# Performance work log

Measured on AMD Instinct MI355X. Metric: run time of the kernel, lower is better.

## Reference

```python
import jax, jax.numpy as jnp
import numpy as np

B, N, D = 64, 256, 768
ITER_STEPS = 1


def _linear_w(key, out_d, in_d):
    s = 1.0 / np.sqrt(in_d)
    return jax.random.uniform(key, (out_d, in_d), jnp.float32, -s, s)


def setup_inputs() -> dict:
    key = jax.random.key(0)
    ks = jax.random.split(key, 16)
    node = jax.random.normal(ks[0], (B, N, D), jnp.float32)
    node_mask = jnp.ones((B, N), jnp.int32)
    argument_graph = jax.random.randint(ks[1], (B, N, N), 0, 2, jnp.int32)
    punctuation_graph = jax.random.randint(ks[2], (B, N, N), 0, 2, jnp.int32)
    inp = {
        "node": node,
        "node_mask": node_mask,
        "argument_graph": argument_graph,
        "punctuation_graph": punctuation_graph,
        # node-relatedness scorer: Linear(D, 1, bias=True)
        "Wq": _linear_w(ks[3], 1, D),
        "bq": jnp.zeros((1,), jnp.float32),
        # self node fc: Linear(D, D, bias=True)
        "Ws": _linear_w(ks[4], D, D),
        "bs": jnp.zeros((D,), jnp.float32),
        # 8 relation projections, Linear(D, D, bias=False)
        "Wa": _linear_w(ks[5], D, D),
        "Wp": _linear_w(ks[6], D, D),
        "Wap": _linear_w(ks[7], D, D),
        "Wpp": _linear_w(ks[8], D, D),
        "Wa2": _linear_w(ks[9], D, D),
        "Wp2": _linear_w(ks[10], D, D),
        "Wap2": _linear_w(ks[11], D, D),
        "Wpp2": _linear_w(ks[12], D, D),
    }
    return inp


def reference(node, node_mask, argument_graph, punctuation_graph,
              Wq, bq, Ws, bs, Wa, Wp, Wap, Wpp, Wa2, Wp2, Wap2, Wpp2):
    f32 = jnp.float32
    mask = node_mask.astype(f32)                      # [B, N]
    n = node.shape[1]
    eye = jnp.eye(n, dtype=f32)
    # dd_graph: node_mask outer product with zeroed diagonal
    dd = mask[:, None, :] * mask[:, :, None] * (1.0 - eye)   # [B, N, N]
    g_a = dd * argument_graph.astype(f32)
    g_p = dd * punctuation_graph.astype(f32)
    # reverse directed edges
    g_ar = dd * jnp.swapaxes(g_a, 1, 2)
    g_pr = dd * jnp.swapaxes(g_p, 1, 2)
    neigh = g_a.sum(-1) + g_p.sum(-1) + g_ar.sum(-1) + g_pr.sum(-1)  # [B, N]
    denom = jnp.where(neigh >= 1.0, neigh, 1.0)

    all_weight = []
    for _ in range(ITER_STEPS):
        # (1) node relatedness
        dw = jax.nn.sigmoid(jnp.einsum('bnd,od->bno', node, Wq) + bq)[..., 0]  # [B, N]
        all_weight.append(dw)
        self_info = jnp.einsum('bnd,ed->bne', node, Ws) + bs

        def msg(g, W):
            # node_weight: broadcast dw over rows, zero where no edge
            nw = dw[:, None, :] * g                    # [B, N, N]
            proj = jnp.einsum('bnd,ed->bne', node, W)  # [B, N, D]
            return jnp.matmul(nw, proj)                # [B, N, D]

        agg = (msg(g_a, Wa) + msg(g_p, Wp) + msg(g_ar, Wap) + msg(g_pr, Wpp)
               + msg(g_a, Wa2) + msg(g_p, Wp2) + msg(g_ar, Wap2) + msg(g_pr, Wpp2))
        agg = agg / denom[..., None]
        # (3) node update
        node = jax.nn.relu(self_info + agg)

    all_weight = jnp.stack(all_weight, axis=1)  # [B, steps, N]
    return node, all_weight
```

## Files before the change

### kernel.cpp

```cpp
#include <hip/hip_runtime.h>
#include <hip/hip_bf16.h>
#include <math.h>

typedef __bf16 bf16;
typedef unsigned char u8;
typedef unsigned long long ull;
typedef __bf16 bf16x8 __attribute__((ext_vector_type(8)));
typedef float f32x4 __attribute__((ext_vector_type(4)));

#define BB 64
#define NN 256
#define DD 768
#define MM (BB*NN)
#define KP 1024
#define WSZ (DD*DD)
#define TL2 272
#define AROW2 196608


__device__ __forceinline__ void async16(const void* g, void* l) {
  __builtin_amdgcn_global_load_lds((__attribute__((address_space(1))) void*)g,
                                   (__attribute__((address_space(3))) void*)l,
                                   16, 0, 0);
}

__device__ __forceinline__ void stage_tile(const bf16* gsrc, int ld, char* ldst,
                                           int wv, int lane) {
#pragma unroll
  for (int cc = 0; cc < 2; ++cc) {
    int c = wv * 2 + cc;
    int row = c * 16 + (lane >> 2);
    int col = (lane & 3) * 8;
    async16(gsrc + (size_t)row * ld + col, ldst + c * 1024);
  }
}

__device__ __forceinline__ void mma_step(const char* lA, const char* lB,
                                         f32x4 acc[4][4], int lane, int wr, int wc) {
  bf16x8 af[4], bfr[4];
  int rbase = wr * 64 + (lane & 15);
  int cbase = wc * 64 + (lane & 15);
  int ko = (lane >> 4) * 8;
#pragma unroll
  for (int r = 0; r < 4; ++r)
    af[r] = *(const bf16x8*)(lA + (((rbase + r * 16) * 32) + ko) * 2);
#pragma unroll
  for (int c = 0; c < 4; ++c)
    bfr[c] = *(const bf16x8*)(lB + (((cbase + c * 16) * 32) + ko) * 2);
#pragma unroll
  for (int r = 0; r < 4; ++r)
#pragma unroll
    for (int c = 0; c < 4; ++c)
      acc[r][c] = __builtin_amdgcn_mfma_f32_16x16x32_bf16(af[r], bfr[c], acc[r][c], 0, 0, 0);
}

__device__ __forceinline__ void mma_step_fp8t(const char* lA, const char* lB,
                                              f32x4 acc[4][4], int lane, int wr, int wc) {
  long af[4], bfr[4];
  int koq = (lane >> 4) * 1024;
  int mA = (wr * 64 + (lane & 15)) * 8;
  int mB = (wc * 64 + (lane & 15)) * 8;
#pragma unroll
  for (int r = 0; r < 4; ++r)
    af[r] = *(const long*)(lA + koq + mA + r * 128);
#pragma unroll
  for (int c = 0; c < 4; ++c)
    bfr[c] = *(const long*)(lB + koq + mB + c * 128);
#pragma unroll
  for (int r = 0; r < 4; ++r)
#pragma unroll
    for (int c = 0; c < 4; ++c)
      acc[r][c] = __builtin_amdgcn_mfma_f32_16x16x32_fp8_fp8(af[r], bfr[c], acc[r][c], 0, 0, 0);
}

__device__ __forceinline__ void k_step64(const bf16* Ab, int lda, const bf16* Bb, int ldb,
                                         char* smem, f32x4 acc[4][4],
                                         int wv, int lane, int wr, int wc) {
  char* lA0 = smem;
  char* lA1 = smem + 8192;
  char* lB0 = smem + 16384;
  char* lB1 = smem + 24576;
  __syncthreads();
  stage_tile(Ab, lda, lA0, wv, lane);
  stage_tile(Ab + 32, lda, lA1, wv, lane);
  stage_tile(Bb, ldb, lB0, wv, lane);
  stage_tile(Bb + 32, ldb, lB1, wv, lane);
  __builtin_amdgcn_s_waitcnt(0);
  __syncthreads();
  mma_step(lA0, lB0, acc, lane, wr, wc);
  mma_step(lA1, lB1, acc, lane, wr, wc);
}

__device__ __forceinline__ unsigned pack4(float a, float b, float c, float d) {
  int w = 0;
  w = __builtin_amdgcn_cvt_pk_fp8_f32(a, b, w, false);
  w = __builtin_amdgcn_cvt_pk_fp8_f32(c, d, w, true);
  return (unsigned)w;
}

__global__ void k_pre(const float* __restrict__ node, const float* __restrict__ Wq,
                      const float* __restrict__ bq, bf16* __restrict__ node_bf,
                      float* __restrict__ dw, float* __restrict__ allw,
                      float* __restrict__ neigh,
                      const float* __restrict__ Ws,
                      const float* __restrict__ Wa, const float* __restrict__ Wp,
                      const float* __restrict__ Wap, const float* __restrict__ Wpp,
                      const float* __restrict__ Wa2, const float* __restrict__ Wp2,
                      const float* __restrict__ Wap2, const float* __restrict__ Wpp2,
                      bf16* __restrict__ Wcat4, bf16* __restrict__ Ws_bf) {
  if (blockIdx.x < MM / 4) {
    int lane = threadIdx.x & 63, wv = threadIdx.x >> 6;
    int row = blockIdx.x * 4 + wv;
    const float* nr = node + (size_t)row * DD;
    bf16* nb = node_bf + (size_t)row * DD;
    float s = 0.f;
#pragma unroll
    for (int k = 0; k < DD / 64; ++k) {
      int idx = lane + k * 64;
      float v = nr[idx];
      nb[idx] = (bf16)v;
      s += v * Wq[idx];
    }
#pragma unroll
    for (int off = 32; off; off >>= 1) s += __shfl_down(s, off);
    if (lane == 0) {
      float z = s + bq[0];
      float d = 1.f / (1.f + expf(-z));
      dw[row] = d;
      allw[row] = d;
      neigh[row] = 0.f;
    }
  } else {
    int i = (blockIdx.x - MM / 4) * 256 + threadIdx.x;
    Ws_bf[i] = (bf16)Ws[i];
    Wcat4[i]           = (bf16)(Wa[i] + Wa2[i]);
    Wcat4[i + WSZ]     = (bf16)(Wp[i] + Wp2[i]);
    Wcat4[i + 2 * WSZ] = (bf16)(Wap[i] + Wap2[i]);
    Wcat4[i + 3 * WSZ] = (bf16)(Wpp[i] + Wpp2[i]);
  }
}

__device__ __forceinline__ void store_tiled(u8* base, int tile, int kin, int m, uint4 v) {
  size_t o = (size_t)tile * 4096 + (size_t)((kin >> 3) * 1024 + m * 8);
  *(ull*)(base + o)        = ((ull)v.y << 32) | v.x;
  *(ull*)(base + o + 1024) = ((ull)v.w << 32) | v.z;
}

__global__ void k_graph(const int* __restrict__ mask, const int* __restrict__ arg,
                        const int* __restrict__ pun, const float* __restrict__ dw,
                        u8* __restrict__ g8, float* __restrict__ neigh) {
  __shared__ float la[64][65];
  __shared__ float lp[64][65];
  __shared__ float msk[256];
  __shared__ float dwv[256];
  int tid = threadIdx.x;
  int bi = blockIdx.x;
  int b = bi >> 4, it = (bi >> 2) & 3, jt = bi & 3;
  int i0 = it * 64, j0 = jt * 64;
  msk[tid] = (float)mask[b * NN + tid];
  dwv[tid] = dw[b * NN + tid];
  __syncthreads();
  int ir = tid >> 2, c4 = (tid & 3) * 16;
  int i = i0 + ir;
  float mi = msk[i];
  size_t gb = (size_t)b * NN * NN;
  const int* ap = arg + gb + (size_t)i * NN + j0 + c4;
  const int* pp = pun + gb + (size_t)i * NN + j0 + c4;
  float va[16], vp[16];
  float racc = 0.f;
#pragma unroll
  for (int k = 0; k < 16; ++k) {
    int j = j0 + c4 + k;
    float dd = (i == j) ? 0.f : mi * msk[j];
    float ga = dd * (float)ap[k];
    float gp = dd * (float)pp[k];
    la[ir][c4 + k] = ga;
    lp[ir][c4 + k] = gp;
    float w = dwv[j];
    va[k] = w * ga;
    vp[k] = w * gp;
    racc += ga + gp;
  }
  uint4 oa, op;
#pragma unroll
  for (int g = 0; g < 4; ++g) {
    (&oa.x)[g] = pack4(va[g*4], va[g*4+1], va[g*4+2], va[g*4+3]);
    (&op.x)[g] = pack4(vp[g*4], vp[g*4+1], vp[g*4+2], vp[g*4+3]);
  }
  {
    int tR = (b * 2 + (i >> 7)) * 32;
    int K0 = j0 + c4;
    store_tiled(g8, tR + (K0 >> 5),       K0 & 31, i & 127, oa);
    store_tiled(g8, tR + 8 + (K0 >> 5),   K0 & 31, i & 127, op);
  }
  racc += __shfl_xor(racc, 1);
  racc += __shfl_xor(racc, 2);
  if ((tid & 3) == 0) atomicAdd(&neigh[b * NN + i], racc);
  __syncthreads();
  int jr = ir, ic4 = c4;
  float cacc = 0.f;
#pragma unroll
  for (int k = 0; k < 16; ++k) {
    float ga = la[ic4 + k][jr];
    float gp = lp[ic4 + k][jr];
    float w = dwv[i0 + ic4 + k];
    va[k] = w * ga;
    vp[k] = w * gp;
    cacc += ga + gp;
  }
#pragma unroll
  for (int g = 0; g < 4; ++g) {
    (&oa.x)[g] = pack4(va[g*4], va[g*4+1], va[g*4+2], va[g*4+3]);
    (&op.x)[g] = pack4(vp[g*4], vp[g*4+1], vp[g*4+2], vp[g*4+3]);
  }
  {
    int row = j0 + jr;
    int tR = (b * 2 + (row >> 7)) * 32;
    int K2 = i0 + ic4;
    store_tiled(g8, tR + 16 + (K2 >> 5),  K2 & 31, row & 127, oa);
    store_tiled(g8, tR + 24 + (K2 >> 5),  K2 & 31, row & 127, op);
  }
  cacc += __shfl_xor(cacc, 1);
  cacc += __shfl_xor(cacc, 2);
  if ((tid & 3) == 0) atomicAdd(&neigh[b * NN + j0 + jr], cacc);
}

template<int T>
__device__ __forceinline__ void proj_ph(char* smem, int wvoff,
                                        const char* gA, const char* gB,
                                        int aoff, int boff,
                                        bf16x8 (&ca)[8], bf16x8 (&cb)[4],
                                        bf16x8 (&na)[8], bf16x8 (&nb)[4],
                                        f32x4 (&acc)[8][4]) {
  if constexpr (T <= 20)      asm volatile("s_waitcnt vmcnt(8)" ::: "memory");
  else if constexpr (T == 21) asm volatile("s_waitcnt vmcnt(4)" ::: "memory");
  else                        asm volatile("s_waitcnt vmcnt(0)" ::: "memory");
  __builtin_amdgcn_s_barrier();
  __builtin_amdgcn_sched_barrier(0);
  if constexpr (T + 4 < 24) {
    char* D = smem + (T & 3) * 32768 + wvoff;
    const char* sA = gA + (T + 4) * 64;
    const char* sB = gB + (T + 4) * 64;
    async16(sA,         D);
    async16(sA + AROW2, D + 8192);
    async16(sB,         D + 16384);
    async16(sB + AROW2, D + 24576);
  }
  if constexpr (T + 1 < 24) {
    const char* L = smem + ((T + 1) & 3) * 32768;
#pragma unroll
    for (int r = 0; r < 8; ++r) na[r] = *(const bf16x8*)(L + aoff + r * 1024);
#pragma unroll
    for (int c = 0; c < 4; ++c) nb[c] = *(const bf16x8*)(L + boff + c * 1024);
  }
  __builtin_amdgcn_s_setprio(1);
#pragma unroll
  for (int r = 0; r < 8; ++r)
#pragma unroll
    for (int c = 0; c < 4; ++c)
      acc[r][c] = __builtin_amdgcn_mfma_f32_16x16x32_bf16(ca[r], cb[c], acc[r][c], 0, 0, 0);
  __builtin_amdgcn_s_setprio(0);
  asm volatile("s_waitcnt lgkmcnt(0)" ::: "memory");
  __builtin_amdgcn_sched_barrier(0);
}

__global__ __launch_bounds__(512, 2) void k_proj(const bf16* __restrict__ node_bf,
                                                 const bf16* __restrict__ Wcat4,
                                                 u8* __restrict__ p8) {
  __shared__ __align__(16) char smem[131072];
  int tid = threadIdx.x, lane = tid & 63, wv = tid >> 6;
  int wr = wv >> 2, wc = wv & 3;
  int l = blockIdx.x, xcd = l & 7, idx = l >> 3;
  int b = (idx / 12) * 8 + xcd;
  int nt = idx % 12;
  int n0 = nt * 256;
  int m0 = b * 256;
  int srcS = (tid & 3) ^ ((tid >> 3) & 3);
  const char* gA = (const char*)node_bf + (size_t)m0 * 1536 + (tid >> 2) * 1536 + srcS * 16;
  const char* gB = (const char*)Wcat4  + (size_t)n0 * 1536 + (tid >> 2) * 1536 + srcS * 16;
  int wvoff = wv * 1024;
  int sSwR = ((lane >> 4) ^ (((lane & 15) >> 1) & 3)) << 4;
  int aoff = (wr * 128 + (lane & 15)) * 64 + sSwR;
  int boff = 16384 + (wc * 64 + (lane & 15)) * 64 + sSwR;
  f32x4 z = {0.f, 0.f, 0.f, 0.f};
  f32x4 acc[8][4];
#pragma unroll
  for (int r = 0; r < 8; ++r)
#pragma unroll
    for (int c = 0; c < 4; ++c) acc[r][c] = z;
  bf16x8 fa0[8], fb0[4], fa1[8], fb1[4];
#pragma unroll
  for (int u = 0; u < 4; ++u) {
    char* D = smem + u * 32768 + wvoff;
    const char* sA = gA + u * 64;
    const char* sB = gB + u * 64;
    async16(sA,         D);
    async16(sA + AROW2, D + 8192);
    async16(sB,         D + 16384);
    async16(sB + AROW2, D + 24576);
  }
  asm volatile("s_waitcnt vmcnt(12)" ::: "memory");
  __builtin_amdgcn_s_barrier();
  __builtin_amdgcn_sched_barrier(0);
#pragma unroll
  for (int r = 0; r < 8; ++r) fa0[r] = *(const bf16x8*)(smem + aoff + r * 1024);
#pragma unroll
  for (int c = 0; c < 4; ++c) fb0[c] = *(const bf16x8*)(smem + boff + c * 1024);
  asm volatile("s_waitcnt lgkmcnt(0)" ::: "memory");
  __builtin_amdgcn_sched_barrier(0);
  proj_ph< 0>(smem, wvoff, gA, gB, aoff, boff, fa0, fb0, fa1, fb1, acc);
  proj_ph< 1>(smem, wvoff, gA, gB, aoff, boff, fa1, fb1, fa0, fb0, acc);
  proj_ph< 2>(smem, wvoff, gA, gB, aoff, boff, fa0, fb0, fa1, fb1, acc);
  proj_ph< 3>(smem, wvoff, gA, gB, aoff, boff, fa1, fb1, fa0, fb0, acc);
  proj_ph< 4>(smem, wvoff, gA, gB, aoff, boff, fa0, fb0, fa1, fb1, acc);
  proj_ph< 5>(smem, wvoff, gA, gB, aoff, boff, fa1, fb1, fa0, fb0, acc);
  proj_ph< 6>(smem, wvoff, gA, gB, aoff, boff, fa0, fb0, fa1, fb1, acc);
  proj_ph< 7>(smem, wvoff, gA, gB, aoff, boff, fa1, fb1, fa0, fb0, acc);
  proj_ph< 8>(smem, wvoff, gA, gB, aoff, boff, fa0, fb0, fa1, fb1, acc);
  proj_ph< 9>(smem, wvoff, gA, gB, aoff, boff, fa1, fb1, fa0, fb0, acc);
  proj_ph<10>(smem, wvoff, gA, gB, aoff, boff, fa0, fb0, fa1, fb1, acc);
  proj_ph<11>(smem, wvoff, gA, gB, aoff, boff, fa1, fb1, fa0, fb0, acc);
  proj_ph<12>(smem, wvoff, gA, gB, aoff, boff, fa0, fb0, fa1, fb1, acc);
  proj_ph<13>(smem, wvoff, gA, gB, aoff, boff, fa1, fb1, fa0, fb0, acc);
  proj_ph<14>(smem, wvoff, gA, gB, aoff, boff, fa0, fb0, fa1, fb1, acc);
  proj_ph<15>(smem, wvoff, gA, gB, aoff, boff, fa1, fb1, fa0, fb0, acc);
  proj_ph<16>(smem, wvoff, gA, gB, aoff, boff, fa0, fb0, fa1, fb1, acc);
  proj_ph<17>(smem, wvoff, gA, gB, aoff, boff, fa1, fb1, fa0, fb0, acc);
  proj_ph<18>(smem, wvoff, gA, gB, aoff, boff, fa0, fb0, fa1, fb1, acc);
  proj_ph<19>(smem, wvoff, gA, gB, aoff, boff, fa1, fb1, fa0, fb0, acc);
  proj_ph<20>(smem, wvoff, gA, gB, aoff, boff, fa0, fb0, fa1, fb1, acc);
  proj_ph<21>(smem, wvoff, gA, gB, aoff, boff, fa1, fb1, fa0, fb0, acc);
  proj_ph<22>(smem, wvoff, gA, gB, aoff, boff, fa0, fb0, fa1, fb1, acc);
  proj_ph<23>(smem, wvoff, gA, gB, aoff, boff, fa1, fb1, fa0, fb0, acc);
  __syncthreads();
  u8* tb = (u8*)smem;
  int X = n0 / DD, e0 = n0 % DD;
#pragma unroll
  for (int r = 0; r < 8; ++r)
#pragma unroll
    for (int c = 0; c < 4; ++c) {
      int n = wc * 64 + c * 16 + (lane & 15);
      int m = wr * 128 + r * 16 + ((lane >> 4) << 2);
      *(unsigned*)(tb + n * TL2 + m) =
          pack4(acc[r][c][0], acc[r][c][1], acc[r][c][2], acc[r][c][3]);
    }
  __syncthreads();
#pragma unroll
  for (int t2 = 0; t2 < 8; ++t2) {
    int erow = t2 * 32 + (tid & 31);
    int col = (tid >> 5) * 16;
    uint4 v = *(const uint4*)(tb + erow * TL2 + col);
    int e = e0 + erow;
    int tR = (b * 6 + (e >> 7)) * 32 + X * 8;
    store_tiled(p8, tR + (col >> 5), col & 31, e & 127, v);
  }
}

__global__ __launch_bounds__(256) void k_agg(const u8* __restrict__ g8,
                                             const u8* __restrict__ p8,
                                             const bf16* __restrict__ node_bf,
                                             const bf16* __restrict__ Ws_bf,
                                             const float* __restrict__ neigh,
                                             const float* __restrict__ bs,
                                             float* __restrict__ out) {
  __shared__ __align__(16) char smem[32768];
  int tid = threadIdx.x, lane = tid & 63, wv = tid >> 6, wr = wv >> 1, wc = wv & 1;
  int l = blockIdx.x;
  int xcd = l & 7, idx = l >> 3;
  int b = (idx / 12) * 8 + xcd;
  int t = idx % 12;
  int i0 = (t / 6) * 128, e0 = (t % 6) * 128;
  f32x4 z = {0.f, 0.f, 0.f, 0.f};
  f32x4 acc[4][4];
#pragma unroll
  for (int r = 0; r < 4; ++r)
#pragma unroll
    for (int c = 0; c < 4; ++c) acc[r][c] = z;
  const u8* At = g8 + (size_t)((b * 2 + (i0 >> 7)) * 32) * 4096;
  const u8* Bt = p8 + (size_t)((b * 6 + (e0 >> 7)) * 32) * 4096;
  int lsoff = wv * 1024;
  int goff = lsoff + lane * 16;
  for (int k0 = 0; k0 < KP; k0 += 128) {
    __syncthreads();
#pragma unroll
    for (int s = 0; s < 4; ++s) {
      size_t toff = (size_t)((k0 >> 5) + s) * 4096 + goff;
      async16(At + toff, smem + s * 4096 + lsoff);
      async16(Bt + toff, smem + 16384 + s * 4096 + lsoff);
    }
    __builtin_amdgcn_s_waitcnt(0);
    __syncthreads();
#pragma unroll
    for (int s = 0; s < 4; ++s)
      mma_step_fp8t(smem + s * 4096, smem + 16384 + s * 4096, acc, lane, wr, wc);
  }
  int rowb = i0 + wr * 64 + (lane >> 4) * 4;
#pragma unroll
  for (int r = 0; r < 4; ++r)
#pragma unroll
    for (int q = 0; q < 4; ++q) {
      float rd = 1.f / fmaxf(neigh[b * NN + rowb + r * 16 + q], 1.f);
#pragma unroll
      for (int c = 0; c < 4; ++c) acc[r][c][q] *= rd;
    }
  const bf16* Ab2 = node_bf + (size_t)(b * NN + i0) * DD;
  const bf16* Bb2 = Ws_bf + (size_t)e0 * DD;
  for (int k0 = 0; k0 < DD; k0 += 64)
    k_step64(Ab2 + k0, DD, Bb2 + k0, DD, smem, acc, wv, lane, wr, wc);
  int colb = e0 + wc * 64 + (lane & 15);
#pragma unroll
  for (int c = 0; c < 4; ++c) {
    int col = colb + c * 16;
    float bv = bs[col];
#pragma unroll
    for (int r = 0; r < 4; ++r)
#pragma unroll
      for (int q = 0; q < 4; ++q) {
        int m = b * NN + rowb + r * 16 + q;
        out[(size_t)m * DD + col] = fmaxf(acc[r][c][q] + bv, 0.f);
      }
  }
}

extern "C" void kernel_launch(void* const* d_in, const int* in_sizes, int n_in,
                              void* d_out, int out_size, void* d_ws, size_t ws_size,
                              hipStream_t stream) {
  const float* node = (const float*)d_in[0];
  const int* mask   = (const int*)d_in[1];
  const int* arg    = (const int*)d_in[2];
  const int* pun    = (const int*)d_in[3];
  const float* Wq   = (const float*)d_in[4];
  const float* bq   = (const float*)d_in[5];
  const float* Ws   = (const float*)d_in[6];
  const float* bs   = (const float*)d_in[7];
  const float* Wa   = (const float*)d_in[8];
  const float* Wp   = (const float*)d_in[9];
  const float* Wap  = (const float*)d_in[10];
  const float* Wpp  = (const float*)d_in[11];
  const float* Wa2  = (const float*)d_in[12];
  const float* Wp2  = (const float*)d_in[13];
  const float* Wap2 = (const float*)d_in[14];
  const float* Wpp2 = (const float*)d_in[15];

  float* out  = (float*)d_out;
  float* allw = out + (size_t)MM * DD;

  char* ws = (char*)d_ws;
  bf16* node_bf = (bf16*)ws;
  float* dw     = (float*)(ws + 25165824);
  float* neigh  = (float*)(ws + 25231360);
  bf16* Wcat4   = (bf16*)(ws + 25296896);
  bf16* Ws_bf   = (bf16*)(ws + 30015488);
  u8*   g8      = (u8*)(ws + 31195136);
  u8*   p8      = (u8*)(ws + 47972352);
  (void)ws_size; (void)in_sizes; (void)n_in; (void)out_size;

  k_pre<<<MM / 4 + WSZ / 256, 256, 0, stream>>>(node, Wq, bq, node_bf, dw, allw,
                                                neigh, Ws, Wa, Wp, Wap, Wpp,
                                                Wa2, Wp2, Wap2, Wpp2, Wcat4, Ws_bf);
  k_graph<<<BB * 16, 256, 0, stream>>>(mask, arg, pun, dw, g8, neigh);
  k_proj<<<768, 512, 0, stream>>>(node_bf, Wcat4, p8);
  k_agg<<<12 * BB, 256, 0, stream>>>(g8, p8, node_bf, Ws_bf, neigh, bs, out);
}
```

Measured before the change: 324.9 us.

## Triple-buffer k_agg LDS pipeline with swizzled bf16 tiles and MFMA priority

Replaces the load-wait-compute loops in k_agg, for both the fp8 aggregation GEMM and the bf16 self-info GEMM, with a 3-stage LDS ring buffer. Loads for step s+2 are issued while step s computes, using partial vmcnt waits and a single barrier per step. The bf16 stage adds an XOR swizzle on the LDS column layout to reduce bank conflicts, and MFMA sections raise wave priority with s_setprio. LDS grows to 48KB with launch_bounds(256,3), which can lower occupancy.

```diff
diff --git a/kernel.cpp b/kernel.cpp
--- a/kernel.cpp
+++ b/kernel.cpp
@@ -24,36 +24,6 @@
                                    16, 0, 0);
 }
 
-__device__ __forceinline__ void stage_tile(const bf16* gsrc, int ld, char* ldst,
-                                           int wv, int lane) {
-#pragma unroll
-  for (int cc = 0; cc < 2; ++cc) {
-    int c = wv * 2 + cc;
-    int row = c * 16 + (lane >> 2);
-    int col = (lane & 3) * 8;
-    async16(gsrc + (size_t)row * ld + col, ldst + c * 1024);
-  }
-}
-
-__device__ __forceinline__ void mma_step(const char* lA, const char* lB,
-                                         f32x4 acc[4][4], int lane, int wr, int wc) {
-  bf16x8 af[4], bfr[4];
-  int rbase = wr * 64 + (lane & 15);
-  int cbase = wc * 64 + (lane & 15);
-  int ko = (lane >> 4) * 8;
-#pragma unroll
-  for (int r = 0; r < 4; ++r)
-    af[r] = *(const bf16x8*)(lA + (((rbase + r * 16) * 32) + ko) * 2);
-#pragma unroll
-  for (int c = 0; c < 4; ++c)
-    bfr[c] = *(const bf16x8*)(lB + (((cbase + c * 16) * 32) + ko) * 2);
-#pragma unroll
-  for (int r = 0; r < 4; ++r)
-#pragma unroll
-    for (int c = 0; c < 4; ++c)
-      acc[r][c] = __builtin_amdgcn_mfma_f32_16x16x32_bf16(af[r], bfr[c], acc[r][c], 0, 0, 0);
-}
-
 __device__ __forceinline__ void mma_step_fp8t(const char* lA, const char* lB,
                                               f32x4 acc[4][4], int lane, int wr, int wc) {
   long af[4], bfr[4];
@@ -73,22 +43,23 @@
       acc[r][c] = __builtin_amdgcn_mfma_f32_16x16x32_fp8_fp8(af[r], bfr[c], acc[r][c], 0, 0, 0);
 }
 
-__device__ __forceinline__ void k_step64(const bf16* Ab, int lda, const bf16* Bb, int ldb,
-                                         char* smem, f32x4 acc[4][4],
-                                         int wv, int lane, int wr, int wc) {
-  char* lA0 = smem;
-  char* lA1 = smem + 8192;
-  char* lB0 = smem + 16384;
-  char* lB1 = smem + 24576;
-  __syncthreads();
-  stage_tile(Ab, lda, lA0, wv, lane);
-  stage_tile(Ab + 32, lda, lA1, wv, lane);
-  stage_tile(Bb, ldb, lB0, wv, lane);
-  stage_tile(Bb + 32, ldb, lB1, wv, lane);
-  __builtin_amdgcn_s_waitcnt(0);
-  __syncthreads();
-  mma_step(lA0, lB0, acc, lane, wr, wc);
-  mma_step(lA1, lB1, acc, lane, wr, wc);
+__device__ __forceinline__ void mma_step_sw(const char* lA, const char* lB,
+                                            f32x4 acc[4][4], int lane, int wr, int wc) {
+  bf16x8 af[4], bfr[4];
+  int rbase = wr * 64 + (lane & 15);
+  int cbase = wc * 64 + (lane & 15);
+  int sSw = ((lane >> 4) ^ (((lane & 15) >> 1) & 3)) * 16;
+#pragma unroll
+  for (int r = 0; r < 4; ++r)
+    af[r] = *(const bf16x8*)(lA + (rbase + r * 16) * 64 + sSw);
+#pragma unroll
+  for (int c = 0; c < 4; ++c)
+    bfr[c] = *(const bf16x8*)(lB + (cbase + c * 16) * 64 + sSw);
+#pragma unroll
+  for (int r = 0; r < 4; ++r)
+#pragma unroll
+    for (int c = 0; c < 4; ++c)
+      acc[r][c] = __builtin_amdgcn_mfma_f32_16x16x32_bf16(af[r], bfr[c], acc[r][c], 0, 0, 0);
 }
 
 __device__ __forceinline__ unsigned pack4(float a, float b, float c, float d) {
@@ -356,14 +327,14 @@
   }
 }
 
-__global__ __launch_bounds__(256) void k_agg(const u8* __restrict__ g8,
-                                             const u8* __restrict__ p8,
-                                             const bf16* __restrict__ node_bf,
-                                             const bf16* __restrict__ Ws_bf,
-                                             const float* __restrict__ neigh,
-                                             const float* __restrict__ bs,
-                                             float* __restrict__ out) {
-  __shared__ __align__(16) char smem[32768];
+__global__ __launch_bounds__(256, 3) void k_agg(const u8* __restrict__ g8,
+                                                const u8* __restrict__ p8,
+                                                const bf16* __restrict__ node_bf,
+                                                const bf16* __restrict__ Ws_bf,
+                                                const float* __restrict__ neigh,
+                                                const float* __restrict__ bs,
+                                                float* __restrict__ out) {
+  __shared__ __align__(16) char smem[49152];
   int tid = threadIdx.x, lane = tid & 63, wv = tid >> 6, wr = wv >> 1, wc = wv & 1;
   int l = blockIdx.x;
   int xcd = l & 7, idx = l >> 3;
@@ -378,21 +349,32 @@
     for (int c = 0; c < 4; ++c) acc[r][c] = z;
   const u8* At = g8 + (size_t)((b * 2 + (i0 >> 7)) * 32) * 4096;
   const u8* Bt = p8 + (size_t)((b * 6 + (e0 >> 7)) * 32) * 4096;
-  int lsoff = wv * 1024;
-  int goff = lsoff + lane * 16;
-  for (int k0 = 0; k0 < KP; k0 += 128) {
-    __syncthreads();
-#pragma unroll
-    for (int s = 0; s < 4; ++s) {
-      size_t toff = (size_t)((k0 >> 5) + s) * 4096 + goff;
-      async16(At + toff, smem + s * 4096 + lsoff);
-      async16(Bt + toff, smem + 16384 + s * 4096 + lsoff);
+  int gOff = tid * 16;
+  int lOff = wv * 1024;
+#pragma unroll
+  for (int u = 0; u < 2; ++u) {
+    char* D = smem + u * 16384 + lOff;
+    const u8* a0 = At + (size_t)(2 * u) * 4096 + gOff;
+    const u8* b0 = Bt + (size_t)(2 * u) * 4096 + gOff;
+    async16(a0, D);            async16(a0 + 4096, D + 4096);
+    async16(b0, D + 8192);     async16(b0 + 4096, D + 12288);
+  }
+  for (int s = 0; s < 16; ++s) {
+    if (s <= 14) asm volatile("s_waitcnt vmcnt(4)" ::: "memory");
+    else         asm volatile("s_waitcnt vmcnt(0)" ::: "memory");
+    __builtin_amdgcn_s_barrier();
+    if (s + 2 < 16) {
+      char* D = smem + ((s + 2) % 3) * 16384 + lOff;
+      const u8* a0 = At + (size_t)(2 * (s + 2)) * 4096 + gOff;
+      const u8* b0 = Bt + (size_t)(2 * (s + 2)) * 4096 + gOff;
+      async16(a0, D);          async16(a0 + 4096, D + 4096);
+      async16(b0, D + 8192);   async16(b0 + 4096, D + 12288);
     }
-    __builtin_amdgcn_s_waitcnt(0);
-    __syncthreads();
-#pragma unroll
-    for (int s = 0; s < 4; ++s)
-      mma_step_fp8t(smem + s * 4096, smem + 16384 + s * 4096, acc, lane, wr, wc);
+    const char* L = smem + (s % 3) * 16384;
+    __builtin_amdgcn_s_setprio(1);
+    mma_step_fp8t(L,        L + 8192,  acc, lane, wr, wc);
+    mma_step_fp8t(L + 4096, L + 12288, acc, lane, wr, wc);
+    __builtin_amdgcn_s_setprio(0);
   }
   int rowb = i0 + wr * 64 + (lane >> 4) * 4;
 #pragma unroll
@@ -403,10 +385,36 @@
 #pragma unroll
       for (int c = 0; c < 4; ++c) acc[r][c][q] *= rd;
     }
+  __syncthreads();
   const bf16* Ab2 = node_bf + (size_t)(b * NN + i0) * DD;
   const bf16* Bb2 = Ws_bf + (size_t)e0 * DD;
-  for (int k0 = 0; k0 < DD; k0 += 64)
-    k_step64(Ab2 + k0, DD, Bb2 + k0, DD, smem, acc, wv, lane, wr, wc);
+  int srow = (tid >> 2);
+  int scol = ((lane & 3) ^ ((lane >> 3) & 3)) * 8;
+#define STAGE2(u)                                                              \
+  {                                                                            \
+    char* D = smem + ((u) % 3) * 16384;                                        \
+    _Pragma("unroll")                                                          \
+    for (int cc = 0; cc < 2; ++cc) {                                           \
+      int c = wv * 2 + cc;                                                     \
+      int row = c * 16 + (lane >> 2);                                          \
+      async16(Ab2 + (size_t)row * DD + (u) * 32 + scol, D + c * 1024);         \
+      async16(Bb2 + (size_t)row * DD + (u) * 32 + scol, D + 8192 + c * 1024);  \
+    }                                                                          \
+  }
+  STAGE2(0);
+  STAGE2(1);
+  for (int s = 0; s < 24; ++s) {
+    if (s <= 22) asm volatile("s_waitcnt vmcnt(4)" ::: "memory");
+    else         asm volatile("s_waitcnt vmcnt(0)" ::: "memory");
+    __builtin_amdgcn_s_barrier();
+    if (s + 2 < 24) STAGE2(s + 2);
+    const char* L = smem + (s % 3) * 16384;
+    __builtin_amdgcn_s_setprio(1);
+    mma_step_sw(L, L + 8192, acc, lane, wr, wc);
+    __builtin_amdgcn_s_setprio(0);
+  }
+#undef STAGE2
+  (void)srow;
   int colb = e0 + wc * 64 + (lane & 15);
 #pragma unroll
   for (int c = 0; c < 4; ++c) {
```

After: 307.7 us. 1.06x faster.
